# Kernel optimization log

Measured on AMD Instinct MI355X. Metric: run time of the kernel, lower is better.

Reference implementation:

```python
import jax, jax.numpy as jnp
import numpy as np

N, E, D, L = 100000, 640000, 128, 5
BN_EPS = 1e-5


def setup_inputs() -> dict:
    key = jax.random.key(0)
    ks = jax.random.split(key, 10)
    x = jax.random.normal(ks[0], (N, D), jnp.float32)
    edge_index = jax.random.randint(ks[1], (2, E), 0, N, dtype=jnp.int32)
    W1 = jax.random.normal(ks[2], (L, D, 2 * D), jnp.float32) / np.float32(np.sqrt(D))
    b1 = jnp.zeros((L, 2 * D), jnp.float32)
    bn1_g = jnp.ones((L, 2 * D), jnp.float32)
    bn1_b = jnp.zeros((L, 2 * D), jnp.float32)
    bn1_m = 0.1 * jax.random.normal(ks[3], (L, 2 * D), jnp.float32)
    bn1_v = jax.random.uniform(ks[4], (L, 2 * D), jnp.float32) + 0.5
    W2 = jax.random.normal(ks[5], (L, 2 * D, D), jnp.float32) / np.float32(np.sqrt(2 * D))
    b2 = jnp.zeros((L, D), jnp.float32)
    bno_g = jnp.ones((L, D), jnp.float32)
    bno_b = jnp.zeros((L, D), jnp.float32)
    bno_m = 0.1 * jax.random.normal(ks[6], (L, D), jnp.float32)
    bno_v = jax.random.uniform(ks[7], (L, D), jnp.float32) + 0.5
    return {"x": x, "edge_index": edge_index, "W1": W1, "b1": b1,
            "bn1_g": bn1_g, "bn1_b": bn1_b, "bn1_m": bn1_m, "bn1_v": bn1_v,
            "W2": W2, "b2": b2,
            "bno_g": bno_g, "bno_b": bno_b, "bno_m": bno_m, "bno_v": bno_v}


def _bn(z, g, b, m, v):
    # BatchNorm1d in eval mode: running stats
    return (z - m) * jax.lax.rsqrt(v + BN_EPS) * g + b


def reference(x, edge_index, W1, b1, bn1_g, bn1_b, bn1_m, bn1_v,
              W2, b2, bno_g, bno_b, bno_m, bno_v):
    src, dst = edge_index[0], edge_index[1]
    h = x
    for l in range(L):
        # GINConv with eps=0: (1+eps)*h_i + sum_{j->i} h_j
        agg = h + jax.ops.segment_sum(h[src], dst, num_segments=N)  # [N, d]
        z = jax.nn.relu(_bn(agg @ W1[l] + b1[l], bn1_g[l], bn1_b[l], bn1_m[l], bn1_v[l]))
        h = _bn(z @ W2[l] + b2[l], bno_g[l], bno_b[l], bno_m[l], bno_v[l])
        if l != L - 1:
            h = jax.nn.relu(h)
        # dropout is identity in eval mode
    return h
```

## Files before the change

kernel.cpp:

```cpp
#include <hip/hip_runtime.h>

#define ND 100000
#define DD 128
#define HH 256
#define EE 640000
#define LL 5

typedef __attribute__((ext_vector_type(8))) short short8;
typedef __attribute__((ext_vector_type(4))) short short4v;
typedef __attribute__((ext_vector_type(4))) float f32x4;

static __device__ __forceinline__ short f2bf(float f) {
    unsigned u = __builtin_bit_cast(unsigned, f);
    unsigned r = (u + 0x7fffu + ((u >> 16) & 1u)) >> 16;
    return (short)r;
}
static __device__ __forceinline__ float bf2f(short s) {
    unsigned u = ((unsigned)(unsigned short)s) << 16;
    return __builtin_bit_cast(float, u);
}

__global__ __launch_bounds__(256) void prep(
    const float* __restrict__ W1, const float* __restrict__ b1,
    const float* __restrict__ g1, const float* __restrict__ bb1,
    const float* __restrict__ m1, const float* __restrict__ v1,
    const float* __restrict__ W2, const float* __restrict__ b2,
    const float* __restrict__ g2, const float* __restrict__ bb2,
    const float* __restrict__ m2, const float* __restrict__ v2,
    short* __restrict__ W1p, float* __restrict__ b1e,
    short* __restrict__ W2p, float* __restrict__ b2e)
{
    int id = blockIdx.x * 256 + threadIdx.x;
    if (id < LL * HH * DD) {
        int l = id >> 15;
        int rem = id & 32767;
        {
            int n = rem >> 7, k = rem & 127;
            float s = g1[l * HH + n] * rsqrtf(v1[l * HH + n] + 1e-5f);
            W1p[id] = f2bf(W1[l * 32768 + k * HH + n] * s);
        }
        {
            int n2 = rem >> 8, k2 = rem & 255;
            float s = g2[l * DD + n2] * rsqrtf(v2[l * DD + n2] + 1e-5f);
            W2p[id] = f2bf(W2[l * 32768 + k2 * DD + n2] * s);
        }
    }
    if (id < LL * HH) {
        float s = g1[id] * rsqrtf(v1[id] + 1e-5f);
        b1e[id] = (b1[id] - m1[id]) * s + bb1[id];
    }
    if (id < LL * DD) {
        float s = g2[id] * rsqrtf(v2[id] + 1e-5f);
        b2e[id] = (b2[id] - m2[id]) * s + bb2[id];
    }
}

__global__ __launch_bounds__(256) void conv_x(const float* __restrict__ x,
                                              short* __restrict__ hb)
{
    int i = blockIdx.x * 256 + threadIdx.x;
    float4 v = reinterpret_cast<const float4*>(x)[i];
    short4v s;
    s.x = f2bf(v.x); s.y = f2bf(v.y); s.z = f2bf(v.z); s.w = f2bf(v.w);
    reinterpret_cast<short4v*>(hb)[i] = s;
}

__global__ __launch_bounds__(256) void zero_counts(int* __restrict__ p)
{
    int i = blockIdx.x * 256 + threadIdx.x;
    if (i * 4 < 2 * ND) {
        int rem = 2 * ND - i * 4;
        if (rem >= 4) reinterpret_cast<int4*>(p)[i] = make_int4(0, 0, 0, 0);
        else for (int j = 0; j < rem; ++j) p[i * 4 + j] = 0;
    }
}

__global__ __launch_bounds__(256) void hist(const int* __restrict__ dst, int* __restrict__ cnt)
{
    int e = blockIdx.x * 256 + threadIdx.x;
    if (e < EE) atomicAdd(&cnt[dst[e]], 1);
}

__global__ __launch_bounds__(256) void scan_block(int* __restrict__ cnt, int* __restrict__ bsum)
{
    __shared__ int buf[256];
    int tid = threadIdx.x;
    int idx = blockIdx.x * 256 + tid;
    int v = (idx < ND) ? cnt[idx] : 0;
    buf[tid] = v;
    __syncthreads();
    int sum = v;
    for (int off = 1; off < 256; off <<= 1) {
        int t = (tid >= off) ? buf[tid - off] : 0;
        __syncthreads();
        sum += t;
        buf[tid] = sum;
        __syncthreads();
    }
    if (idx < ND) cnt[idx] = sum;
    if (tid == 255) bsum[blockIdx.x] = sum;
}

__global__ __launch_bounds__(512) void scan_bsum(const int* __restrict__ bsum,
                                                 int* __restrict__ boffs)
{
    __shared__ int buf[512];
    int tid = threadIdx.x;
    int v = (tid < 391) ? bsum[tid] : 0;
    buf[tid] = v;
    __syncthreads();
    int sum = v;
    for (int off = 1; off < 512; off <<= 1) {
        int t = (tid >= off) ? buf[tid - off] : 0;
        __syncthreads();
        sum += t;
        buf[tid] = sum;
        __syncthreads();
    }
    if (tid < 391) boffs[tid] = sum - v;
}

__global__ __launch_bounds__(256) void apply_offs(const int* __restrict__ cnt,
                                                  const int* __restrict__ boffs,
                                                  int* __restrict__ rowst)
{
    int idx = blockIdx.x * 256 + threadIdx.x;
    if (idx < ND) rowst[idx + 1] = cnt[idx] + boffs[blockIdx.x];
    if (idx == 0) rowst[0] = 0;
}

__global__ __launch_bounds__(256) void fill_csr(const int* __restrict__ src,
                                                const int* __restrict__ dst,
                                                const int* __restrict__ rowstart,
                                                int* __restrict__ cursor,
                                                int* __restrict__ csr)
{
    int e = blockIdx.x * 256 + threadIdx.x;
    if (e < EE) {
        int d = dst[e];
        int p = atomicAdd(&cursor[d], 1);
        csr[rowstart[d] + p] = src[e];
    }
}

__global__ __launch_bounds__(256) void agg_gather(const short* __restrict__ hb,
                                                  const int* __restrict__ rowstart,
                                                  const int* __restrict__ csr,
                                                  short* __restrict__ aggb)
{
    int g = blockIdx.x * 256 + threadIdx.x;
    int node = g >> 4;
    if (node >= ND) return;
    int c = (g & 15) * 8;
    int s = rowstart[node], e = rowstart[node + 1];
    float acc[8];
    {
        short8 h0 = *reinterpret_cast<const short8*>(&hb[(size_t)node * DD + c]);
        for (int j = 0; j < 8; ++j) acc[j] = bf2f(h0[j]);
    }
    int i = s;
    for (; i + 1 < e; i += 2) {
        int s0 = csr[i], s1 = csr[i + 1];
        short8 a = *reinterpret_cast<const short8*>(&hb[(size_t)s0 * DD + c]);
        short8 b = *reinterpret_cast<const short8*>(&hb[(size_t)s1 * DD + c]);
        for (int j = 0; j < 8; ++j) acc[j] += bf2f(a[j]) + bf2f(b[j]);
    }
    if (i < e) {
        int s0 = csr[i];
        short8 a = *reinterpret_cast<const short8*>(&hb[(size_t)s0 * DD + c]);
        for (int j = 0; j < 8; ++j) acc[j] += bf2f(a[j]);
    }
    short8 o;
    for (int j = 0; j < 8; ++j) o[j] = f2bf(acc[j]);
    *reinterpret_cast<short8*>(&aggb[(size_t)node * DD + c]) = o;
}

__global__ __launch_bounds__(256, 4) void mlp(
    const short* __restrict__ aggb,
    const short* __restrict__ W1l,
    const float* __restrict__ b1l,
    const short* __restrict__ W2l,
    const float* __restrict__ b2l,
    short* __restrict__ hb_out, float* __restrict__ f_out, int last)
{
    __shared__ __attribute__((aligned(16))) short sU[64 * 264];

    const int tid = threadIdx.x;
    const int r0 = blockIdx.x * 64;
    const int wave = tid >> 6;
    const int lane = tid & 63;
    const int quad = lane >> 4;
    const int l16 = lane & 15;

    for (int p = 0; p < 4; ++p) {
        int linear = p * 256 + tid;
        int row = linear >> 4;
        int ch = (linear & 15) * 8;
        int grow = r0 + row;
        short8 v;
        if (grow < ND) v = *reinterpret_cast<const short8*>(&aggb[(size_t)grow * DD + ch]);
        else for (int j = 0; j < 8; ++j) v[j] = 0;
        *reinterpret_cast<short8*>(&sU[row * 136 + ch]) = v;
    }
    __syncthreads();

    const f32x4 zero4 = {0.f, 0.f, 0.f, 0.f};
    f32x4 acc1[4][4];
    for (int rt = 0; rt < 4; ++rt)
        for (int ct = 0; ct < 4; ++ct) acc1[rt][ct] = zero4;

    const int cbase = wave * 64;
    for (int ks = 0; ks < 4; ++ks) {
        int kofs = ks * 32 + quad * 8;
        short8 a[4], b[4];
        for (int ct = 0; ct < 4; ++ct)
            b[ct] = *reinterpret_cast<const short8*>(&W1l[(cbase + ct * 16 + l16) * DD + kofs]);
        for (int rt = 0; rt < 4; ++rt)
            a[rt] = *reinterpret_cast<const short8*>(&sU[(rt * 16 + l16) * 136 + kofs]);
        for (int rt = 0; rt < 4; ++rt)
            for (int ct = 0; ct < 4; ++ct)
                acc1[rt][ct] = __builtin_amdgcn_mfma_f32_16x16x32_bf16(
                    a[rt], b[ct], acc1[rt][ct], 0, 0, 0);
    }
    __syncthreads();

    for (int ct = 0; ct < 4; ++ct) {
        int col = cbase + ct * 16 + l16;
        float bias = b1l[col];
        for (int rt = 0; rt < 4; ++rt) {
            for (int r = 0; r < 4; ++r) {
                int row = rt * 16 + quad * 4 + r;
                float v = acc1[rt][ct][r] + bias;
                v = fmaxf(v, 0.f);
                sU[row * 264 + col] = f2bf(v);
            }
        }
    }
    __syncthreads();

    f32x4 acc2[4][2];
    for (int rt = 0; rt < 4; ++rt)
        for (int ct = 0; ct < 2; ++ct) acc2[rt][ct] = zero4;

    const int c2 = wave * 32;
    for (int ks = 0; ks < 8; ++ks) {
        int kofs = ks * 32 + quad * 8;
        short8 a[4], b[2];
        for (int ct = 0; ct < 2; ++ct)
            b[ct] = *reinterpret_cast<const short8*>(&W2l[(c2 + ct * 16 + l16) * HH + kofs]);
        for (int rt = 0; rt < 4; ++rt)
            a[rt] = *reinterpret_cast<const short8*>(&sU[(rt * 16 + l16) * 264 + kofs]);
        for (int rt = 0; rt < 4; ++rt)
            for (int ct = 0; ct < 2; ++ct)
                acc2[rt][ct] = __builtin_amdgcn_mfma_f32_16x16x32_bf16(
                    a[rt], b[ct], acc2[rt][ct], 0, 0, 0);
    }

    for (int ct = 0; ct < 2; ++ct) {
        int col = c2 + ct * 16 + l16;
        float bias = b2l[col];
        for (int rt = 0; rt < 4; ++rt) {
            for (int r = 0; r < 4; ++r) {
                int grow = r0 + rt * 16 + quad * 4 + r;
                if (grow < ND) {
                    float v = acc2[rt][ct][r] + bias;
                    if (!last) {
                        v = fmaxf(v, 0.f);
                        hb_out[(size_t)grow * DD + col] = f2bf(v);
                    } else {
                        f_out[(size_t)grow * DD + col] = v;
                    }
                }
            }
        }
    }
}

extern "C" void kernel_launch(void* const* d_in, const int* in_sizes, int n_in,
                              void* d_out, int out_size, void* d_ws, size_t ws_size,
                              hipStream_t stream)
{
    const float* x  = (const float*)d_in[0];
    const int* ei   = (const int*)d_in[1];
    const int* src  = ei;
    const int* dst  = ei + EE;
    const float* W1 = (const float*)d_in[2];
    const float* b1 = (const float*)d_in[3];
    const float* g1 = (const float*)d_in[4];
    const float* bb1= (const float*)d_in[5];
    const float* m1 = (const float*)d_in[6];
    const float* v1 = (const float*)d_in[7];
    const float* W2 = (const float*)d_in[8];
    const float* b2 = (const float*)d_in[9];
    const float* g2 = (const float*)d_in[10];
    const float* bb2= (const float*)d_in[11];
    const float* m2 = (const float*)d_in[12];
    const float* v2 = (const float*)d_in[13];

    char* w = (char*)d_ws;
    short* aggb  = (short*)w;
    short* hbuf  = (short*)(w + 25600000);
    short* W1p   = (short*)(w + 51200000);
    short* W2p   = (short*)(w + 51527680);
    float* b1e   = (float*)(w + 51855360);
    float* b2e   = (float*)(w + 51860480);
    int*   cnt   = (int*)  (w + 51863040);
    int*   cursor= (int*)  (w + 52263040);
    int*   rowst = (int*)  (w + 52663040);
    int*   csr   = (int*)  (w + 53063072);
    int*   bsum  = (int*)  (w + 55623072);
    int*   boffs = (int*)  (w + 55624736);
    float* out   = (float*)d_out;

    prep<<<640, 256, 0, stream>>>(W1, b1, g1, bb1, m1, v1,
                                  W2, b2, g2, bb2, m2, v2,
                                  W1p, b1e, W2p, b2e);
    zero_counts<<<196, 256, 0, stream>>>(cnt);
    hist<<<2500, 256, 0, stream>>>(dst, cnt);
    scan_block<<<391, 256, 0, stream>>>(cnt, bsum);
    scan_bsum<<<1, 512, 0, stream>>>(bsum, boffs);
    apply_offs<<<391, 256, 0, stream>>>(cnt, boffs, rowst);
    fill_csr<<<2500, 256, 0, stream>>>(src, dst, rowst, cursor, csr);
    conv_x<<<12500, 256, 0, stream>>>(x, hbuf);

    for (int l = 0; l < LL; ++l) {
        agg_gather<<<6250, 256, 0, stream>>>(hbuf, rowst, csr, aggb);
        mlp<<<1563, 256, 0, stream>>>(aggb,
                                      W1p + l * 32768, b1e + l * HH,
                                      W2p + l * 32768, b2e + l * DD,
                                      hbuf, out, (l == LL - 1) ? 1 : 0);
    }
}
```

Baseline: 573.6 us.

## Fuse neighbor aggregation into MLP kernel and merge setup kernels

The per-layer gather kernel is folded into the MLP kernel: each block aggregates its 64 rows straight into shared memory, so the bf16 agg buffer no longer makes a round trip through global memory. Ping-pong h buffers replace in-place updates. The weight prep, x conversion and histogram kernels are merged into one launch. The MMA operands are swapped so each lane writes four consecutive output columns, which allows vectorized stores. The fused gather has lower parallelism per row (16 threads per row inside 256-thread blocks with launch bounds of 4), which may hurt the latency hiding that the gather phase relies on.

```diff
diff --git a/kernel.cpp b/kernel.cpp
--- a/kernel.cpp
+++ b/kernel.cpp
@@ -20,49 +20,54 @@
     return __builtin_bit_cast(float, u);
 }
 
-__global__ __launch_bounds__(256) void prep(
+__global__ __launch_bounds__(256) void setup(
     const float* __restrict__ W1, const float* __restrict__ b1,
     const float* __restrict__ g1, const float* __restrict__ bb1,
     const float* __restrict__ m1, const float* __restrict__ v1,
     const float* __restrict__ W2, const float* __restrict__ b2,
     const float* __restrict__ g2, const float* __restrict__ bb2,
     const float* __restrict__ m2, const float* __restrict__ v2,
+    const float* __restrict__ x, const int* __restrict__ dst,
     short* __restrict__ W1p, float* __restrict__ b1e,
-    short* __restrict__ W2p, float* __restrict__ b2e)
-{
-    int id = blockIdx.x * 256 + threadIdx.x;
-    if (id < LL * HH * DD) {
-        int l = id >> 15;
-        int rem = id & 32767;
-        {
-            int n = rem >> 7, k = rem & 127;
-            float s = g1[l * HH + n] * rsqrtf(v1[l * HH + n] + 1e-5f);
-            W1p[id] = f2bf(W1[l * 32768 + k * HH + n] * s);
-        }
-        {
-            int n2 = rem >> 8, k2 = rem & 255;
-            float s = g2[l * DD + n2] * rsqrtf(v2[l * DD + n2] + 1e-5f);
-            W2p[id] = f2bf(W2[l * 32768 + k2 * DD + n2] * s);
-        }
-    }
-    if (id < LL * HH) {
-        float s = g1[id] * rsqrtf(v1[id] + 1e-5f);
-        b1e[id] = (b1[id] - m1[id]) * s + bb1[id];
-    }
-    if (id < LL * DD) {
-        float s = g2[id] * rsqrtf(v2[id] + 1e-5f);
-        b2e[id] = (b2[id] - m2[id]) * s + bb2[id];
-    }
-}
-
-__global__ __launch_bounds__(256) void conv_x(const float* __restrict__ x,
-                                              short* __restrict__ hb)
-{
-    int i = blockIdx.x * 256 + threadIdx.x;
-    float4 v = reinterpret_cast<const float4*>(x)[i];
-    short4v s;
-    s.x = f2bf(v.x); s.y = f2bf(v.y); s.z = f2bf(v.z); s.w = f2bf(v.w);
-    reinterpret_cast<short4v*>(hb)[i] = s;
+    short* __restrict__ W2p, float* __restrict__ b2e,
+    short* __restrict__ hb, int* __restrict__ cnt)
+{
+    int bx = blockIdx.x;
+    int tid = threadIdx.x;
+    if (bx < 640) {
+        int id = bx * 256 + tid;
+        if (id < LL * HH * DD) {
+            int l = id >> 15;
+            int rem = id & 32767;
+            {
+                int n = rem >> 7, k = rem & 127;
+                float s = g1[l * HH + n] * rsqrtf(v1[l * HH + n] + 1e-5f);
+                W1p[id] = f2bf(W1[l * 32768 + k * HH + n] * s);
+            }
+            {
+                int n2 = rem >> 8, k2 = rem & 255;
+                float s = g2[l * DD + n2] * rsqrtf(v2[l * DD + n2] + 1e-5f);
+                W2p[id] = f2bf(W2[l * 32768 + k2 * DD + n2] * s);
+            }
+        }
+        if (id < LL * HH) {
+            float s = g1[id] * rsqrtf(v1[id] + 1e-5f);
+            b1e[id] = (b1[id] - m1[id]) * s + bb1[id];
+        }
+        if (id < LL * DD) {
+            float s = g2[id] * rsqrtf(v2[id] + 1e-5f);
+            b2e[id] = (b2[id] - m2[id]) * s + bb2[id];
+        }
+    } else if (bx < 13140) {
+        int i = (bx - 640) * 256 + tid;
+        float4 v = reinterpret_cast<const float4*>(x)[i];
+        short4v s;
+        s.x = f2bf(v.x); s.y = f2bf(v.y); s.z = f2bf(v.z); s.w = f2bf(v.w);
+        reinterpret_cast<short4v*>(hb)[i] = s;
+    } else {
+        int e = (bx - 13140) * 256 + tid;
+        if (e < EE) atomicAdd(&cnt[dst[e]], 1);
+    }
 }
 
 __global__ __launch_bounds__(256) void zero_counts(int* __restrict__ p)
@@ -73,12 +78,6 @@
         if (rem >= 4) reinterpret_cast<int4*>(p)[i] = make_int4(0, 0, 0, 0);
         else for (int j = 0; j < rem; ++j) p[i * 4 + j] = 0;
     }
-}
-
-__global__ __launch_bounds__(256) void hist(const int* __restrict__ dst, int* __restrict__ cnt)
-{
-    int e = blockIdx.x * 256 + threadIdx.x;
-    if (e < EE) atomicAdd(&cnt[dst[e]], 1);
 }
 
 __global__ __launch_bounds__(256) void scan_block(int* __restrict__ cnt, int* __restrict__ bsum)
@@ -143,40 +142,10 @@
     }
 }
 
-__global__ __launch_bounds__(256) void agg_gather(const short* __restrict__ hb,
-                                                  const int* __restrict__ rowstart,
-                                                  const int* __restrict__ csr,
-                                                  short* __restrict__ aggb)
-{
-    int g = blockIdx.x * 256 + threadIdx.x;
-    int node = g >> 4;
-    if (node >= ND) return;
-    int c = (g & 15) * 8;
-    int s = rowstart[node], e = rowstart[node + 1];
-    float acc[8];
-    {
-        short8 h0 = *reinterpret_cast<const short8*>(&hb[(size_t)node * DD + c]);
-        for (int j = 0; j < 8; ++j) acc[j] = bf2f(h0[j]);
-    }
-    int i = s;
-    for (; i + 1 < e; i += 2) {
-        int s0 = csr[i], s1 = csr[i + 1];
-        short8 a = *reinterpret_cast<const short8*>(&hb[(size_t)s0 * DD + c]);
-        short8 b = *reinterpret_cast<const short8*>(&hb[(size_t)s1 * DD + c]);
-        for (int j = 0; j < 8; ++j) acc[j] += bf2f(a[j]) + bf2f(b[j]);
-    }
-    if (i < e) {
-        int s0 = csr[i];
-        short8 a = *reinterpret_cast<const short8*>(&hb[(size_t)s0 * DD + c]);
-        for (int j = 0; j < 8; ++j) acc[j] += bf2f(a[j]);
-    }
-    short8 o;
-    for (int j = 0; j < 8; ++j) o[j] = f2bf(acc[j]);
-    *reinterpret_cast<short8*>(&aggb[(size_t)node * DD + c]) = o;
-}
-
-__global__ __launch_bounds__(256, 4) void mlp(
-    const short* __restrict__ aggb,
+__global__ __launch_bounds__(256, 4) void layer_fused(
+    const short* __restrict__ hb_in,
+    const int* __restrict__ rowst,
+    const int* __restrict__ csr,
     const short* __restrict__ W1l,
     const float* __restrict__ b1l,
     const short* __restrict__ W2l,
@@ -193,83 +162,108 @@
     const int l16 = lane & 15;
 
     for (int p = 0; p < 4; ++p) {
-        int linear = p * 256 + tid;
-        int row = linear >> 4;
-        int ch = (linear & 15) * 8;
+        int t = p * 256 + tid;
+        int row = t >> 4;
+        int ch = (t & 15) * 8;
         int grow = r0 + row;
-        short8 v;
-        if (grow < ND) v = *reinterpret_cast<const short8*>(&aggb[(size_t)grow * DD + ch]);
-        else for (int j = 0; j < 8; ++j) v[j] = 0;
-        *reinterpret_cast<short8*>(&sU[row * 136 + ch]) = v;
+        float acc[8];
+        if (grow < ND) {
+            short8 h0 = *reinterpret_cast<const short8*>(&hb_in[(size_t)grow * DD + ch]);
+            for (int j = 0; j < 8; ++j) acc[j] = bf2f(h0[j]);
+            int s = rowst[grow], e = rowst[grow + 1];
+            int i = s;
+            for (; i + 1 < e; i += 2) {
+                int s0 = csr[i], s1 = csr[i + 1];
+                short8 a = *reinterpret_cast<const short8*>(&hb_in[(size_t)s0 * DD + ch]);
+                short8 b = *reinterpret_cast<const short8*>(&hb_in[(size_t)s1 * DD + ch]);
+                for (int j = 0; j < 8; ++j) acc[j] += bf2f(a[j]) + bf2f(b[j]);
+            }
+            if (i < e) {
+                short8 a = *reinterpret_cast<const short8*>(&hb_in[(size_t)csr[i] * DD + ch]);
+                for (int j = 0; j < 8; ++j) acc[j] += bf2f(a[j]);
+            }
+        } else {
+            for (int j = 0; j < 8; ++j) acc[j] = 0.f;
+        }
+        short8 o;
+        for (int j = 0; j < 8; ++j) o[j] = f2bf(acc[j]);
+        *reinterpret_cast<short8*>(&sU[row * 136 + ch]) = o;
     }
     __syncthreads();
 
     const f32x4 zero4 = {0.f, 0.f, 0.f, 0.f};
     f32x4 acc1[4][4];
-    for (int rt = 0; rt < 4; ++rt)
-        for (int ct = 0; ct < 4; ++ct) acc1[rt][ct] = zero4;
-
-    const int cbase = wave * 64;
+    for (int mt = 0; mt < 4; ++mt)
+        for (int nt = 0; nt < 4; ++nt) acc1[mt][nt] = zero4;
+
+    const int wb = wave * 64;
     for (int ks = 0; ks < 4; ++ks) {
         int kofs = ks * 32 + quad * 8;
-        short8 a[4], b[4];
-        for (int ct = 0; ct < 4; ++ct)
-            b[ct] = *reinterpret_cast<const short8*>(&W1l[(cbase + ct * 16 + l16) * DD + kofs]);
-        for (int rt = 0; rt < 4; ++rt)
-            a[rt] = *reinterpret_cast<const short8*>(&sU[(rt * 16 + l16) * 136 + kofs]);
-        for (int rt = 0; rt < 4; ++rt)
-            for (int ct = 0; ct < 4; ++ct)
-                acc1[rt][ct] = __builtin_amdgcn_mfma_f32_16x16x32_bf16(
-                    a[rt], b[ct], acc1[rt][ct], 0, 0, 0);
-    }
-    __syncthreads();
-
-    for (int ct = 0; ct < 4; ++ct) {
-        int col = cbase + ct * 16 + l16;
-        float bias = b1l[col];
-        for (int rt = 0; rt < 4; ++rt) {
-            for (int r = 0; r < 4; ++r) {
-                int row = rt * 16 + quad * 4 + r;
-                float v = acc1[rt][ct][r] + bias;
-                v = fmaxf(v, 0.f);
-                sU[row * 264 + col] = f2bf(v);
-            }
-        }
-    }
-    __syncthreads();
-
-    f32x4 acc2[4][2];
-    for (int rt = 0; rt < 4; ++rt)
-        for (int ct = 0; ct < 2; ++ct) acc2[rt][ct] = zero4;
+        short8 aw[4], bn[4];
+        for (int mt = 0; mt < 4; ++mt)
+            aw[mt] = *reinterpret_cast<const short8*>(&W1l[(wb + mt * 16 + l16) * DD + kofs]);
+        for (int nt = 0; nt < 4; ++nt)
+            bn[nt] = *reinterpret_cast<const short8*>(&sU[(nt * 16 + l16) * 136 + kofs]);
+        for (int mt = 0; mt < 4; ++mt)
+            for (int nt = 0; nt < 4; ++nt)
+                acc1[mt][nt] = __builtin_amdgcn_mfma_f32_16x16x32_bf16(
+                    aw[mt], bn[nt], acc1[mt][nt], 0, 0, 0);
+    }
+    __syncthreads();
+
+    for (int mt = 0; mt < 4; ++mt) {
+        int zc = wb + mt * 16 + quad * 4;
+        float4 bias = *reinterpret_cast<const float4*>(&b1l[zc]);
+        for (int nt = 0; nt < 4; ++nt) {
+            int node = nt * 16 + l16;
+            short4v o;
+            o.x = f2bf(fmaxf(acc1[mt][nt][0] + bias.x, 0.f));
+            o.y = f2bf(fmaxf(acc1[mt][nt][1] + bias.y, 0.f));
+            o.z = f2bf(fmaxf(acc1[mt][nt][2] + bias.z, 0.f));
+            o.w = f2bf(fmaxf(acc1[mt][nt][3] + bias.w, 0.f));
+            *reinterpret_cast<short4v*>(&sU[node * 264 + zc]) = o;
+        }
+    }
+    __syncthreads();
+
+    f32x4 acc2[2][4];
+    for (int ct = 0; ct < 2; ++ct)
+        for (int nt = 0; nt < 4; ++nt) acc2[ct][nt] = zero4;
 
     const int c2 = wave * 32;
     for (int ks = 0; ks < 8; ++ks) {
         int kofs = ks * 32 + quad * 8;
-        short8 a[4], b[2];
+        short8 aw[2], bn[4];
         for (int ct = 0; ct < 2; ++ct)
-            b[ct] = *reinterpret_cast<const short8*>(&W2l[(c2 + ct * 16 + l16) * HH + kofs]);
-        for (int rt = 0; rt < 4; ++rt)
-            a[rt] = *reinterpret_cast<const short8*>(&sU[(rt * 16 + l16) * 264 + kofs]);
-        for (int rt = 0; rt < 4; ++rt)
-            for (int ct = 0; ct < 2; ++ct)
-                acc2[rt][ct] = __builtin_amdgcn_mfma_f32_16x16x32_bf16(
-                    a[rt], b[ct], acc2[rt][ct], 0, 0, 0);
+            aw[ct] = *reinterpret_cast<const short8*>(&W2l[(c2 + ct * 16 + l16) * HH + kofs]);
+        for (int nt = 0; nt < 4; ++nt)
+            bn[nt] = *reinterpret_cast<const short8*>(&sU[(nt * 16 + l16) * 264 + kofs]);
+        for (int ct = 0; ct < 2; ++ct)
+            for (int nt = 0; nt < 4; ++nt)
+                acc2[ct][nt] = __builtin_amdgcn_mfma_f32_16x16x32_bf16(
+                    aw[ct], bn[nt], acc2[ct][nt], 0, 0, 0);
     }
 
     for (int ct = 0; ct < 2; ++ct) {
-        int col = c2 + ct * 16 + l16;
-        float bias = b2l[col];
-        for (int rt = 0; rt < 4; ++rt) {
-            for (int r = 0; r < 4; ++r) {
-                int grow = r0 + rt * 16 + quad * 4 + r;
-                if (grow < ND) {
-                    float v = acc2[rt][ct][r] + bias;
-                    if (!last) {
-                        v = fmaxf(v, 0.f);
-                        hb_out[(size_t)grow * DD + col] = f2bf(v);
-                    } else {
-                        f_out[(size_t)grow * DD + col] = v;
-                    }
+        int oc = c2 + ct * 16 + quad * 4;
+        float4 bias = *reinterpret_cast<const float4*>(&b2l[oc]);
+        for (int nt = 0; nt < 4; ++nt) {
+            int node = r0 + nt * 16 + l16;
+            if (node < ND) {
+                float v0 = acc2[ct][nt][0] + bias.x;
+                float v1 = acc2[ct][nt][1] + bias.y;
+                float v2 = acc2[ct][nt][2] + bias.z;
+                float v3 = acc2[ct][nt][3] + bias.w;
+                if (!last) {
+                    short4v o;
+                    o.x = f2bf(fmaxf(v0, 0.f));
+                    o.y = f2bf(fmaxf(v1, 0.f));
+                    o.z = f2bf(fmaxf(v2, 0.f));
+                    o.w = f2bf(fmaxf(v3, 0.f));
+                    *reinterpret_cast<short4v*>(&hb_out[(size_t)node * DD + oc]) = o;
+                } else {
+                    float4 st; st.x = v0; st.y = v1; st.z = v2; st.w = v3;
+                    *reinterpret_cast<float4*>(&f_out[(size_t)node * DD + oc]) = st;
                 }
             }
         }
@@ -298,8 +292,8 @@
     const float* v2 = (const float*)d_in[13];
 
     char* w = (char*)d_ws;
-    short* aggb  = (short*)w;
-    short* hbuf  = (short*)(w + 25600000);
+    short* hbufA = (short*)w;
+    short* hbufB = (short*)(w + 25600000);
     short* W1p   = (short*)(w + 51200000);
     short* W2p   = (short*)(w + 51527680);
     float* b1e   = (float*)(w + 51855360);
@@ -312,22 +306,22 @@
     int*   boffs = (int*)  (w + 55624736);
     float* out   = (float*)d_out;
 
-    prep<<<640, 256, 0, stream>>>(W1, b1, g1, bb1, m1, v1,
-                                  W2, b2, g2, bb2, m2, v2,
-                                  W1p, b1e, W2p, b2e);
     zero_counts<<<196, 256, 0, stream>>>(cnt);
-    hist<<<2500, 256, 0, stream>>>(dst, cnt);
+    setup<<<15640, 256, 0, stream>>>(W1, b1, g1, bb1, m1, v1,
+                                     W2, b2, g2, bb2, m2, v2,
+                                     x, dst, W1p, b1e, W2p, b2e, hbufA, cnt);
     scan_block<<<391, 256, 0, stream>>>(cnt, bsum);
     scan_bsum<<<1, 512, 0, stream>>>(bsum, boffs);
     apply_offs<<<391, 256, 0, stream>>>(cnt, boffs, rowst);
     fill_csr<<<2500, 256, 0, stream>>>(src, dst, rowst, cursor, csr);
-    conv_x<<<12500, 256, 0, stream>>>(x, hbuf);
-
+
+    short* hin = hbufA;
+    short* hout = hbufB;
     for (int l = 0; l < LL; ++l) {
-        agg_gather<<<6250, 256, 0, stream>>>(hbuf, rowst, csr, aggb);
-        mlp<<<1563, 256, 0, stream>>>(aggb,
-                                      W1p + l * 32768, b1e + l * HH,
-                                      W2p + l * 32768, b2e + l * DD,
-                                      hbuf, out, (l == LL - 1) ? 1 : 0);
-    }
-}
+        layer_fused<<<1563, 256, 0, stream>>>(hin, rowst, csr,
+                                              W1p + l * 32768, b1e + l * HH,
+                                              W2p + l * 32768, b2e + l * DD,
+                                              hout, out, (l == LL - 1) ? 1 : 0);
+        short* t = hin; hin = hout; hout = t;
+    }
+}
```

New measurement: 555.7 us. 3.1% less time.
